# Optimization experiments

Measured on AMD Instinct MI355X. Metric: run time of the kernel, lower is better.

The kernel has to match this reference:

```python
import jax, jax.numpy as jnp
import numpy as np


def setup_inputs() -> dict:
    key = jax.random.key(0)
    ks = jax.random.split(key, 8)
    B, L, D, N, K = 4, 4096, 1024, 64, 4
    return {
        "x": jax.random.normal(ks[0], (B, L, D), dtype=jnp.float32),
        "conv_w": jax.random.normal(ks[1], (K, 1, D), dtype=jnp.float32) * 0.1,
        "conv_b": jnp.zeros((D,), dtype=jnp.float32),
        "Wp": jax.random.normal(ks[2], (D, 2 * N), dtype=jnp.float32) * (1.0 / np.sqrt(D)),
        "bp": jnp.zeros((2 * N,), dtype=jnp.float32),
        "Ws": jax.random.normal(ks[3], (D, N), dtype=jnp.float32) * (1.0 / np.sqrt(D)),
        "bs": jnp.zeros((N,), dtype=jnp.float32),
        "A_log": jax.random.normal(ks[4], (N,), dtype=jnp.float32) * 0.02,
        "dt_log": jax.random.normal(ks[5], (N,), dtype=jnp.float32) * 0.02,
        "Wo": jax.random.normal(ks[6], (N, D), dtype=jnp.float32) * (1.0 / np.sqrt(N)),
        "bo": jnp.zeros((D,), dtype=jnp.float32),
    }


def reference(x, conv_w, conv_b, Wp, bp, Ws, bs, A_log, dt_log, Wo, bo):
    B, L, D = x.shape
    K = conv_w.shape[0]
    N = Ws.shape[1]

    # causal depthwise conv: left-pad by K-1, sum K shifted slices (K is tiny)
    x_pad = jnp.pad(x, ((0, 0), (K - 1, 0), (0, 0)))
    conv = conv_b + sum(x_pad[:, k:k + L, :] * conv_w[k, 0] for k in range(K))

    proj = conv @ Wp + bp                     # [B, L, 2N]
    B_t = jax.nn.softplus(proj[..., :N])      # [B, L, N]
    C_t = jnp.tanh(proj[..., N:])             # [B, L, N]
    u = x @ Ws + bs                           # [B, L, N]

    A = -jax.nn.softplus(A_log)               # [N]
    dt = jax.nn.softplus(dt_log)              # [N]
    decay = 1.0 + dt * A                      # [N]

    def step(state, inputs):
        u_t, b_t, c_t = inputs                # each [B, N]
        state = decay * state + dt * b_t * u_t
        return state, c_t * state

    init = jnp.zeros((B, N), dtype=x.dtype)
    xs = tuple(jnp.swapaxes(a, 0, 1) for a in (u, B_t, C_t))  # time-major
    _, ys = jax.lax.scan(step, init, xs, unroll=4)            # [L, B, N]
    y = jnp.swapaxes(ys, 0, 1)                                # [B, L, N]
    return y @ Wo + bo                                        # [B, L, D]
```

## Files before the change

### kernel.cpp

```cpp
#include <hip/hip_runtime.h>

#define B_ 4
#define L_ 4096
#define D_ 1024
#define N_ 64

typedef _Float16 f16;
typedef __attribute__((ext_vector_type(8))) _Float16 half8;
typedef __attribute__((ext_vector_type(4))) float f32x4;

__device__ __forceinline__ float softplus_f(float x) {
    return fmaxf(x, 0.0f) + log1pf(__expf(-fabsf(x)));
}

__device__ __forceinline__ float tanh_f(float x) {
    float xc = fminf(fmaxf(x, -15.0f), 15.0f);
    float e = __expf(2.0f * xc);
    return (e - 1.0f) / (e + 1.0f);
}

__global__ __launch_bounds__(256) void k_prepw(
    const float* __restrict__ Wp, const float* __restrict__ Ws,
    const float* __restrict__ Wo, f16* __restrict__ WT, f16* __restrict__ WoT)
{
    int gid = blockIdx.x * 256 + threadIdx.x;
    if (gid < 24576) {
        int r = gid >> 7, kg = gid & 127;
        const float* src; int ncol, c;
        if (r < 128) { src = Wp; ncol = 128; c = r; }
        else         { src = Ws; ncol = 64;  c = r - 128; }
        f16 h[8];
        #pragma unroll
        for (int j = 0; j < 8; j++)
            h[j] = (f16)src[(size_t)(kg * 8 + j) * ncol + c];
        *(uint4*)&WT[(size_t)r * 1024 + kg * 8] = *(uint4*)h;
    } else {
        int g2 = gid - 24576;
        int d = g2 >> 3, ng = g2 & 7;
        f16 h[8];
        #pragma unroll
        for (int j = 0; j < 8; j++)
            h[j] = (f16)Wo[(size_t)(ng * 8 + j) * D_ + d];
        *(uint4*)&WoT[(size_t)d * 64 + ng * 8] = *(uint4*)h;
    }
}

__global__ __launch_bounds__(256) void k_frontend(
    const float* __restrict__ x, const float* __restrict__ conv_w,
    const float* __restrict__ conv_b, const f16* __restrict__ WT,
    const float* __restrict__ bp, const float* __restrict__ bs,
    const float* __restrict__ dt_log,
    f16* __restrict__ zT, f16* __restrict__ cT)
{
    __shared__ __align__(16) f16 xh[36 * 72];
    __shared__ float sE[3 * 32 * 68];

    const int tid = threadIdx.x;
    const int w = tid >> 6, lane = tid & 63;
    const int r = lane & 15, q = lane >> 4;
    const int T0 = blockIdx.x * 32;
    const int bb = T0 >> 12;
    const int l0 = T0 & (L_ - 1);
    const int cw0 = w * 48;

    f32x4 acc[3][2] = {};
    float4 rA[3];

    #define LDX(c0)                                                          \
        {                                                                    \
            _Pragma("unroll")                                                \
            for (int s = 0; s < 3; s++) {                                    \
                int idx = tid + 256 * s;                                     \
                float4 v = make_float4(0.f, 0.f, 0.f, 0.f);                  \
                if (idx < 576) {                                             \
                    int row = idx >> 4, g = idx & 15;                        \
                    int l = l0 + row - 4;                                    \
                    if (l >= 0)                                              \
                        v = *(const float4*)&x[((size_t)(bb * L_ + l)) * D_  \
                                               + (c0) + g * 4];              \
                }                                                            \
                rA[s] = v;                                                   \
            }                                                                \
        }

    LDX(0);
    for (int c = 0; c < 16; c++) {
        __syncthreads();
        #pragma unroll
        for (int s = 0; s < 3; s++) {
            int idx = tid + 256 * s;
            if (idx < 576) {
                int row = idx >> 4, g = idx & 15;
                f16 h[4] = {(f16)rA[s].x, (f16)rA[s].y, (f16)rA[s].z, (f16)rA[s].w};
                *(uint2*)&xh[row * 72 + g * 4] = *(uint2*)h;
            }
        }
        __syncthreads();
        if (c < 15) LDX((c + 1) * 64);

        const int k0 = c * 64;
        #pragma unroll
        for (int ks = 0; ks < 2; ks++) {
            const int kk = k0 + ks * 32 + q * 8;
            const int kl = ks * 32 + q * 8;

            half8 af[3];
            #pragma unroll
            for (int mf = 0; mf < 3; mf++)
                af[mf] = *(const half8*)&WT[(size_t)(cw0 + mf * 16 + r) * 1024 + kk];

            float cw3[8], cw2[8], cw1[8], cw0v[8], cbv[8];
            if (w < 3) {
                float4 a0 = *(const float4*)&conv_w[3 * D_ + kk];
                float4 a1 = *(const float4*)&conv_w[3 * D_ + kk + 4];
                float4 b0 = *(const float4*)&conv_w[2 * D_ + kk];
                float4 b1 = *(const float4*)&conv_w[2 * D_ + kk + 4];
                float4 c0v = *(const float4*)&conv_w[1 * D_ + kk];
                float4 c1v = *(const float4*)&conv_w[1 * D_ + kk + 4];
                float4 d0v = *(const float4*)&conv_w[0 * D_ + kk];
                float4 d1v = *(const float4*)&conv_w[0 * D_ + kk + 4];
                float4 e0 = *(const float4*)&conv_b[kk];
                float4 e1 = *(const float4*)&conv_b[kk + 4];
                cw3[0]=a0.x;cw3[1]=a0.y;cw3[2]=a0.z;cw3[3]=a0.w;cw3[4]=a1.x;cw3[5]=a1.y;cw3[6]=a1.z;cw3[7]=a1.w;
                cw2[0]=b0.x;cw2[1]=b0.y;cw2[2]=b0.z;cw2[3]=b0.w;cw2[4]=b1.x;cw2[5]=b1.y;cw2[6]=b1.z;cw2[7]=b1.w;
                cw1[0]=c0v.x;cw1[1]=c0v.y;cw1[2]=c0v.z;cw1[3]=c0v.w;cw1[4]=c1v.x;cw1[5]=c1v.y;cw1[6]=c1v.z;cw1[7]=c1v.w;
                cw0v[0]=d0v.x;cw0v[1]=d0v.y;cw0v[2]=d0v.z;cw0v[3]=d0v.w;cw0v[4]=d1v.x;cw0v[5]=d1v.y;cw0v[6]=d1v.z;cw0v[7]=d1v.w;
                cbv[0]=e0.x;cbv[1]=e0.y;cbv[2]=e0.z;cbv[3]=e0.w;cbv[4]=e1.x;cbv[5]=e1.y;cbv[6]=e1.z;cbv[7]=e1.w;
            }

            half8 braw[2], bcnv[2];
            #pragma unroll
            for (int nf = 0; nf < 2; nf++) {
                const int rb = nf * 16 + r + 4;
                half8 h0 = *(const half8*)&xh[rb * 72 + kl];
                braw[nf] = h0;
                if (w < 3) {
                    half8 h1 = *(const half8*)&xh[(rb - 1) * 72 + kl];
                    half8 h2 = *(const half8*)&xh[(rb - 2) * 72 + kl];
                    half8 h3 = *(const half8*)&xh[(rb - 3) * 72 + kl];
                    half8 hc;
                    #pragma unroll
                    for (int u = 0; u < 8; u++) {
                        float s0 = cbv[u];
                        s0 = fmaf(cw3[u], (float)h0[u], s0);
                        s0 = fmaf(cw2[u], (float)h1[u], s0);
                        s0 = fmaf(cw1[u], (float)h2[u], s0);
                        s0 = fmaf(cw0v[u], (float)h3[u], s0);
                        hc[u] = (f16)s0;
                    }
                    bcnv[nf] = hc;
                }
            }

            #pragma unroll
            for (int mf = 0; mf < 3; mf++) {
                const bool useConv = (cw0 + mf * 16) < 128;
                #pragma unroll
                for (int nf = 0; nf < 2; nf++)
                    acc[mf][nf] = __builtin_amdgcn_mfma_f32_16x16x32_f16(
                        af[mf], useConv ? bcnv[nf] : braw[nf], acc[mf][nf], 0, 0, 0);
            }
        }
    }

    float* sB = sE;
    float* sC = sE + 32 * 68;
    float* sU = sE + 2 * 32 * 68;
    __syncthreads();
    #pragma unroll
    for (int mf = 0; mf < 3; mf++) {
        const int cb4 = cw0 + mf * 16 + q * 4;
        const int seg = cb4 >> 6;
        const int cl = cb4 & 63;
        const float4 bb4 = (seg == 2) ? *(const float4*)&bs[cl]
                                      : *(const float4*)&bp[cb4];
        float* dst = (seg == 0) ? sB : (seg == 1 ? sC : sU);
        #pragma unroll
        for (int nf = 0; nf < 2; nf++) {
            const int t = nf * 16 + r;
            float v0 = acc[mf][nf][0] + bb4.x;
            float v1 = acc[mf][nf][1] + bb4.y;
            float v2 = acc[mf][nf][2] + bb4.z;
            float v3 = acc[mf][nf][3] + bb4.w;
            if (seg == 0) {
                v0 = softplus_f(v0); v1 = softplus_f(v1);
                v2 = softplus_f(v2); v3 = softplus_f(v3);
            } else if (seg == 1) {
                v0 = tanh_f(v0); v1 = tanh_f(v1);
                v2 = tanh_f(v2); v3 = tanh_f(v3);
            }
            float4 vv = {v0, v1, v2, v3};
            *(float4*)&dst[t * 68 + cl] = vv;
        }
    }
    __syncthreads();

    {
        const int n = tid >> 2, tg = tid & 3;
        const float dtv = softplus_f(dt_log[n]);
        f16 hz[8], hc[8];
        #pragma unroll
        for (int j = 0; j < 8; j++) {
            const int t = tg * 8 + j;
            hz[j] = (f16)(dtv * sB[t * 68 + n] * sU[t * 68 + n]);
            hc[j] = (f16)sC[t * 68 + n];
        }
        size_t o = ((size_t)(bb * N_ + n)) * L_ + l0 + tg * 8;
        *(uint4*)&zT[o] = *(uint4*)hz;
        *(uint4*)&cT[o] = *(uint4*)hc;
    }
    #undef LDX
}

__global__ __launch_bounds__(64) void k_scan(
    const f16* __restrict__ zT, const f16* __restrict__ cT,
    const float* __restrict__ A_log, const float* __restrict__ dt_log,
    f16* __restrict__ yH)
{
    __shared__ float zs[L_];
    __shared__ float cs[L_];
    const int bn = blockIdx.x;
    const int n = bn & (N_ - 1);
    const int lane = threadIdx.x;
    const f16* zp = zT + (size_t)bn * L_;
    const f16* cp = cT + (size_t)bn * L_;

    for (int it = 0; it < 8; it++) {
        int i = lane * 8 + it * 512;
        uint4 rz = *(const uint4*)(zp + i);
        uint4 rc = *(const uint4*)(cp + i);
        const f16* hz = (const f16*)&rz;
        const f16* hc = (const f16*)&rc;
        #pragma unroll
        for (int k = 0; k < 8; k++) {
            zs[i + k] = (float)hz[k];
            cs[i + k] = (float)hc[k];
        }
    }
    __syncthreads();

    float dtv = softplus_f(dt_log[n]);
    float Av = -softplus_f(A_log[n]);
    float dec = fmaf(dtv, Av, 1.0f);

    float s = 0.0f;
    const int base = lane * 64;
    #pragma unroll
    for (int j = 0; j < 64; j++) s = fmaf(dec, s, zs[base + j]);

    float d2 = dec * dec, d4 = d2 * d2, d8 = d4 * d4;
    float d16 = d8 * d8, d32 = d16 * d16, d64 = d32 * d32;

    float Ag = d64, Bg = s;
    #pragma unroll
    for (int off = 1; off < 64; off <<= 1) {
        float Ap = __shfl_up(Ag, off);
        float Bp = __shfl_up(Bg, off);
        if (lane >= off) { Bg = fmaf(Ag, Bp, Bg); Ag *= Ap; }
    }
    float carry = __shfl_up(Bg, 1);
    if (lane == 0) carry = 0.0f;

    float st = carry;
    #pragma unroll
    for (int j = 0; j < 64; j++) {
        st = fmaf(dec, st, zs[base + j]);
        zs[base + j] = cs[base + j] * st;
    }
    __syncthreads();
    f16* yp = yH + (size_t)bn * L_;
    for (int i = lane * 8; i < L_; i += 512) {
        f16 h[8];
        #pragma unroll
        for (int k = 0; k < 8; k++) h[k] = (f16)zs[i + k];
        *(uint4*)&yp[i] = *(uint4*)h;
    }
}

__global__ __launch_bounds__(256) void k_out(
    const f16* __restrict__ yH, const f16* __restrict__ WoT,
    const float* __restrict__ bo, float* __restrict__ out)
{
    __shared__ __align__(16) f16 ys[64 * 72];
    const int tid = threadIdx.x;
    const int w = tid >> 6, lane = tid & 63;
    const int r = lane & 15, q = lane >> 4;
    const int T0 = blockIdx.x * 64;
    const int bb = T0 >> 12, l0 = T0 & (L_ - 1);
    const int dw = blockIdx.y * 128 + w * 32;

    {
        const int n = tid & 63, tg = tid >> 6;
        #pragma unroll
        for (int h2 = 0; h2 < 2; h2++) {
            uint4 v = *(const uint4*)&yH[((size_t)(bb * N_ + n)) * L_ + l0 + tg * 16 + h2 * 8];
            const f16* hh = (const f16*)&v;
            #pragma unroll
            for (int j = 0; j < 8; j++)
                ys[(tg * 16 + h2 * 8 + j) * 72 + n] = hh[j];
        }
    }
    __syncthreads();

    f32x4 acc[2][4] = {};
    #pragma unroll
    for (int ks = 0; ks < 2; ks++) {
        const int kk = ks * 32 + q * 8;
        half8 af[2];
        #pragma unroll
        for (int mf = 0; mf < 2; mf++)
            af[mf] = *(const half8*)&WoT[(size_t)(dw + mf * 16 + r) * 64 + kk];
        #pragma unroll
        for (int nf = 0; nf < 4; nf++) {
            half8 bf = *(const half8*)&ys[(nf * 16 + r) * 72 + kk];
            #pragma unroll
            for (int mf = 0; mf < 2; mf++)
                acc[mf][nf] = __builtin_amdgcn_mfma_f32_16x16x32_f16(
                    af[mf], bf, acc[mf][nf], 0, 0, 0);
        }
    }

    #pragma unroll
    for (int mf = 0; mf < 2; mf++) {
        const int d = dw + mf * 16 + q * 4;
        const float4 bb4 = *(const float4*)&bo[d];
        #pragma unroll
        for (int nf = 0; nf < 4; nf++) {
            const int t = T0 + nf * 16 + r;
            float4 o = {acc[mf][nf][0] + bb4.x, acc[mf][nf][1] + bb4.y,
                        acc[mf][nf][2] + bb4.z, acc[mf][nf][3] + bb4.w};
            *(float4*)&out[(size_t)t * D_ + d] = o;
        }
    }
}

extern "C" void kernel_launch(void* const* d_in, const int* in_sizes, int n_in,
                              void* d_out, int out_size, void* d_ws, size_t ws_size,
                              hipStream_t stream) {
    const float* x      = (const float*)d_in[0];
    const float* conv_w = (const float*)d_in[1];
    const float* conv_b = (const float*)d_in[2];
    const float* Wp     = (const float*)d_in[3];
    const float* bp     = (const float*)d_in[4];
    const float* Ws     = (const float*)d_in[5];
    const float* bs     = (const float*)d_in[6];
    const float* A_log  = (const float*)d_in[7];
    const float* dt_log = (const float*)d_in[8];
    const float* Wo     = (const float*)d_in[9];
    const float* bo     = (const float*)d_in[10];
    float* out = (float*)d_out;

    char* wsp = (char*)d_ws;
    f16* WT  = (f16*)wsp;
    f16* WoT = (f16*)(wsp + 393216);
    f16* zT  = (f16*)(wsp + 524288);
    f16* cT  = (f16*)(wsp + 2621440);
    f16* yH  = (f16*)(wsp + 4718592);

    k_prepw<<<dim3(128), dim3(256), 0, stream>>>(Wp, Ws, Wo, WT, WoT);
    k_frontend<<<dim3(B_ * L_ / 32), dim3(256), 0, stream>>>(
        x, conv_w, conv_b, WT, bp, bs, dt_log, zT, cT);
    k_scan<<<dim3(B_ * N_), dim3(64), 0, stream>>>(zT, cT, A_log, dt_log, yH);
    k_out<<<dim3(B_ * L_ / 64, D_ / 128), dim3(256), 0, stream>>>(yH, WoT, bo, out);
}
```

Baseline: 201.2 us.

## Double-buffer frontend tiles, precompute conv once, parallelize scan across four waves

The frontend kernel now stages conv weights in shared memory. It computes the causal conv once per tile into a shared buffer instead of redundantly per wave, double-buffers the x tile, and prefetches weight fragments for the next chunk into registers. The scan kernel moves from one 64-thread wave with shared-memory staging to 256 threads that each hold 16 elements in registers, combining wave totals with a two-level parallel scan. The output kernel hoists its Wo fragment loads before the shared-memory staging. The changes add shared-memory and register pressure and raise the risk of precision loss in the powered decay terms.

```diff
diff --git a/kernel.cpp b/kernel.cpp
--- a/kernel.cpp
+++ b/kernel.cpp
@@ -52,7 +52,10 @@
     const float* __restrict__ dt_log,
     f16* __restrict__ zT, f16* __restrict__ cT)
 {
-    __shared__ __align__(16) f16 xh[36 * 72];
+    __shared__ float cwS[4 * 1024];
+    __shared__ float cbS[1024];
+    __shared__ __align__(16) f16 xh[2][36 * 72];
+    __shared__ __align__(16) f16 cvh[32 * 72];
     __shared__ float sE[3 * 32 * 68];
 
     const int tid = threadIdx.x;
@@ -65,6 +68,7 @@
 
     f32x4 acc[3][2] = {};
     float4 rA[3];
+    half8 wt[2][3][2];
 
     #define LDX(c0)                                                          \
         {                                                                    \
@@ -83,90 +87,111 @@
             }                                                                \
         }
 
+    #define STX(buf)                                                         \
+        {                                                                    \
+            _Pragma("unroll")                                                \
+            for (int s = 0; s < 3; s++) {                                    \
+                int idx = tid + 256 * s;                                     \
+                if (idx < 576) {                                             \
+                    int row = idx >> 4, g = idx & 15;                        \
+                    f16 h[4] = {(f16)rA[s].x, (f16)rA[s].y,                  \
+                                (f16)rA[s].z, (f16)rA[s].w};                 \
+                    *(uint2*)&xh[buf][row * 72 + g * 4] = *(uint2*)h;        \
+                }                                                            \
+            }                                                                \
+        }
+
+    #define LDWT(buf, cc)                                                    \
+        {                                                                    \
+            const int kb = (cc) * 64;                                        \
+            _Pragma("unroll")                                                \
+            for (int mf = 0; mf < 3; mf++)                                   \
+                _Pragma("unroll")                                            \
+                for (int ks = 0; ks < 2; ks++)                               \
+                    wt[buf][mf][ks] = *(const half8*)&WT[                    \
+                        (size_t)(cw0 + mf * 16 + r) * 1024 + kb + ks * 32 +  \
+                        q * 8];                                              \
+        }
+
+    for (int idx = tid; idx < 1024; idx += 256)
+        *(float4*)&cwS[idx * 4] = *(const float4*)&conv_w[idx * 4];
+    for (int idx = tid; idx < 256; idx += 256)
+        *(float4*)&cbS[idx * 4] = *(const float4*)&conv_b[idx * 4];
+
     LDX(0);
+    STX(0);
+    LDX(64);
+    LDWT(0, 0);
+    __syncthreads();
+
     for (int c = 0; c < 16; c++) {
+        const int cur = c & 1;
+        {
+            const int t = tid >> 3, kg = tid & 7;
+            const int kb = c * 64 + kg * 8;
+            float4 w3a = *(const float4*)&cwS[3 * 1024 + kb];
+            float4 w3b = *(const float4*)&cwS[3 * 1024 + kb + 4];
+            float4 w2a = *(const float4*)&cwS[2 * 1024 + kb];
+            float4 w2b = *(const float4*)&cwS[2 * 1024 + kb + 4];
+            float4 w1a = *(const float4*)&cwS[1 * 1024 + kb];
+            float4 w1b = *(const float4*)&cwS[1 * 1024 + kb + 4];
+            float4 w0a = *(const float4*)&cwS[0 * 1024 + kb];
+            float4 w0b = *(const float4*)&cwS[0 * 1024 + kb + 4];
+            float4 cba = *(const float4*)&cbS[kb];
+            float4 cbb = *(const float4*)&cbS[kb + 4];
+            half8 x0 = *(const half8*)&xh[cur][(t + 4) * 72 + kg * 8];
+            half8 x1 = *(const half8*)&xh[cur][(t + 3) * 72 + kg * 8];
+            half8 x2 = *(const half8*)&xh[cur][(t + 2) * 72 + kg * 8];
+            half8 x3 = *(const half8*)&xh[cur][(t + 1) * 72 + kg * 8];
+            float w3v[8] = {w3a.x,w3a.y,w3a.z,w3a.w,w3b.x,w3b.y,w3b.z,w3b.w};
+            float w2v[8] = {w2a.x,w2a.y,w2a.z,w2a.w,w2b.x,w2b.y,w2b.z,w2b.w};
+            float w1v[8] = {w1a.x,w1a.y,w1a.z,w1a.w,w1b.x,w1b.y,w1b.z,w1b.w};
+            float w0v[8] = {w0a.x,w0a.y,w0a.z,w0a.w,w0b.x,w0b.y,w0b.z,w0b.w};
+            float cbv[8] = {cba.x,cba.y,cba.z,cba.w,cbb.x,cbb.y,cbb.z,cbb.w};
+            half8 hc;
+            #pragma unroll
+            for (int u = 0; u < 8; u++) {
+                float s0 = cbv[u];
+                s0 = fmaf(w3v[u], (float)x0[u], s0);
+                s0 = fmaf(w2v[u], (float)x1[u], s0);
+                s0 = fmaf(w1v[u], (float)x2[u], s0);
+                s0 = fmaf(w0v[u], (float)x3[u], s0);
+                hc[u] = (f16)s0;
+            }
+            *(uint4*)&cvh[t * 72 + kg * 8] = *(uint4*)&hc;
+        }
         __syncthreads();
-        #pragma unroll
-        for (int s = 0; s < 3; s++) {
-            int idx = tid + 256 * s;
-            if (idx < 576) {
-                int row = idx >> 4, g = idx & 15;
-                f16 h[4] = {(f16)rA[s].x, (f16)rA[s].y, (f16)rA[s].z, (f16)rA[s].w};
-                *(uint2*)&xh[row * 72 + g * 4] = *(uint2*)h;
-            }
-        }
-        __syncthreads();
-        if (c < 15) LDX((c + 1) * 64);
-
-        const int k0 = c * 64;
+
+        if (c < 15) LDWT(1 - cur, c + 1);
+
         #pragma unroll
         for (int ks = 0; ks < 2; ks++) {
-            const int kk = k0 + ks * 32 + q * 8;
             const int kl = ks * 32 + q * 8;
-
-            half8 af[3];
-            #pragma unroll
-            for (int mf = 0; mf < 3; mf++)
-                af[mf] = *(const half8*)&WT[(size_t)(cw0 + mf * 16 + r) * 1024 + kk];
-
-            float cw3[8], cw2[8], cw1[8], cw0v[8], cbv[8];
-            if (w < 3) {
-                float4 a0 = *(const float4*)&conv_w[3 * D_ + kk];
-                float4 a1 = *(const float4*)&conv_w[3 * D_ + kk + 4];
-                float4 b0 = *(const float4*)&conv_w[2 * D_ + kk];
-                float4 b1 = *(const float4*)&conv_w[2 * D_ + kk + 4];
-                float4 c0v = *(const float4*)&conv_w[1 * D_ + kk];
-                float4 c1v = *(const float4*)&conv_w[1 * D_ + kk + 4];
-                float4 d0v = *(const float4*)&conv_w[0 * D_ + kk];
-                float4 d1v = *(const float4*)&conv_w[0 * D_ + kk + 4];
-                float4 e0 = *(const float4*)&conv_b[kk];
-                float4 e1 = *(const float4*)&conv_b[kk + 4];
-                cw3[0]=a0.x;cw3[1]=a0.y;cw3[2]=a0.z;cw3[3]=a0.w;cw3[4]=a1.x;cw3[5]=a1.y;cw3[6]=a1.z;cw3[7]=a1.w;
-                cw2[0]=b0.x;cw2[1]=b0.y;cw2[2]=b0.z;cw2[3]=b0.w;cw2[4]=b1.x;cw2[5]=b1.y;cw2[6]=b1.z;cw2[7]=b1.w;
-                cw1[0]=c0v.x;cw1[1]=c0v.y;cw1[2]=c0v.z;cw1[3]=c0v.w;cw1[4]=c1v.x;cw1[5]=c1v.y;cw1[6]=c1v.z;cw1[7]=c1v.w;
-                cw0v[0]=d0v.x;cw0v[1]=d0v.y;cw0v[2]=d0v.z;cw0v[3]=d0v.w;cw0v[4]=d1v.x;cw0v[5]=d1v.y;cw0v[6]=d1v.z;cw0v[7]=d1v.w;
-                cbv[0]=e0.x;cbv[1]=e0.y;cbv[2]=e0.z;cbv[3]=e0.w;cbv[4]=e1.x;cbv[5]=e1.y;cbv[6]=e1.z;cbv[7]=e1.w;
-            }
-
             half8 braw[2], bcnv[2];
             #pragma unroll
             for (int nf = 0; nf < 2; nf++) {
-                const int rb = nf * 16 + r + 4;
-                half8 h0 = *(const half8*)&xh[rb * 72 + kl];
-                braw[nf] = h0;
-                if (w < 3) {
-                    half8 h1 = *(const half8*)&xh[(rb - 1) * 72 + kl];
-                    half8 h2 = *(const half8*)&xh[(rb - 2) * 72 + kl];
-                    half8 h3 = *(const half8*)&xh[(rb - 3) * 72 + kl];
-                    half8 hc;
-                    #pragma unroll
-                    for (int u = 0; u < 8; u++) {
-                        float s0 = cbv[u];
-                        s0 = fmaf(cw3[u], (float)h0[u], s0);
-                        s0 = fmaf(cw2[u], (float)h1[u], s0);
-                        s0 = fmaf(cw1[u], (float)h2[u], s0);
-                        s0 = fmaf(cw0v[u], (float)h3[u], s0);
-                        hc[u] = (f16)s0;
-                    }
-                    bcnv[nf] = hc;
-                }
+                braw[nf] = *(const half8*)&xh[cur][(nf * 16 + r + 4) * 72 + kl];
+                bcnv[nf] = *(const half8*)&cvh[(nf * 16 + r) * 72 + kl];
             }
-
             #pragma unroll
             for (int mf = 0; mf < 3; mf++) {
                 const bool useConv = (cw0 + mf * 16) < 128;
                 #pragma unroll
                 for (int nf = 0; nf < 2; nf++)
                     acc[mf][nf] = __builtin_amdgcn_mfma_f32_16x16x32_f16(
-                        af[mf], useConv ? bcnv[nf] : braw[nf], acc[mf][nf], 0, 0, 0);
+                        wt[cur][mf][ks], useConv ? bcnv[nf] : braw[nf],
+                        acc[mf][nf], 0, 0, 0);
             }
         }
+
+        if (c < 15) STX(1 - cur);
+        if (c < 14) LDX((c + 2) * 64);
+        __syncthreads();
     }
 
     float* sB = sE;
     float* sC = sE + 32 * 68;
     float* sU = sE + 2 * 32 * 68;
-    __syncthreads();
     #pragma unroll
     for (int mf = 0; mf < 3; mf++) {
         const int cb4 = cw0 + mf * 16 + q * 4;
@@ -210,71 +235,88 @@
         *(uint4*)&cT[o] = *(uint4*)hc;
     }
     #undef LDX
-}
-
-__global__ __launch_bounds__(64) void k_scan(
+    #undef STX
+    #undef LDWT
+}
+
+__global__ __launch_bounds__(256) void k_scan(
     const f16* __restrict__ zT, const f16* __restrict__ cT,
     const float* __restrict__ A_log, const float* __restrict__ dt_log,
     f16* __restrict__ yH)
 {
-    __shared__ float zs[L_];
-    __shared__ float cs[L_];
+    __shared__ float Tw[4];
     const int bn = blockIdx.x;
     const int n = bn & (N_ - 1);
-    const int lane = threadIdx.x;
-    const f16* zp = zT + (size_t)bn * L_;
-    const f16* cp = cT + (size_t)bn * L_;
-
-    for (int it = 0; it < 8; it++) {
-        int i = lane * 8 + it * 512;
-        uint4 rz = *(const uint4*)(zp + i);
-        uint4 rc = *(const uint4*)(cp + i);
-        const f16* hz = (const f16*)&rz;
-        const f16* hc = (const f16*)&rc;
-        #pragma unroll
-        for (int k = 0; k < 8; k++) {
-            zs[i + k] = (float)hz[k];
-            cs[i + k] = (float)hc[k];
-        }
-    }
-    __syncthreads();
-
-    float dtv = softplus_f(dt_log[n]);
-    float Av = -softplus_f(A_log[n]);
-    float dec = fmaf(dtv, Av, 1.0f);
+    const int tid = threadIdx.x;
+    const int w = tid >> 6, lane = tid & 63;
+    const size_t base = (size_t)bn * L_ + tid * 16;
+
+    uint4 uz0 = *(const uint4*)(zT + base);
+    uint4 uz1 = *(const uint4*)(zT + base + 8);
+    uint4 uc0 = *(const uint4*)(cT + base);
+    uint4 uc1 = *(const uint4*)(cT + base + 8);
+
+    float z[16], cc[16];
+    {
+        const f16* hz0 = (const f16*)&uz0;
+        const f16* hz1 = (const f16*)&uz1;
+        const f16* hc0 = (const f16*)&uc0;
+        const f16* hc1 = (const f16*)&uc1;
+        #pragma unroll
+        for (int j = 0; j < 8; j++) {
+            z[j] = (float)hz0[j]; z[8 + j] = (float)hz1[j];
+            cc[j] = (float)hc0[j]; cc[8 + j] = (float)hc1[j];
+        }
+    }
+
+    const float dtv = softplus_f(dt_log[n]);
+    const float Av = -softplus_f(A_log[n]);
+    const float dec = fmaf(dtv, Av, 1.0f);
 
     float s = 0.0f;
-    const int base = lane * 64;
-    #pragma unroll
-    for (int j = 0; j < 64; j++) s = fmaf(dec, s, zs[base + j]);
-
-    float d2 = dec * dec, d4 = d2 * d2, d8 = d4 * d4;
-    float d16 = d8 * d8, d32 = d16 * d16, d64 = d32 * d32;
-
-    float Ag = d64, Bg = s;
+    #pragma unroll
+    for (int j = 0; j < 16; j++) s = fmaf(dec, s, z[j]);
+
+    const float d2 = dec * dec, d4 = d2 * d2, d8 = d4 * d4, a16 = d8 * d8;
+
+    float Ag = a16, Bg = s;
     #pragma unroll
     for (int off = 1; off < 64; off <<= 1) {
         float Ap = __shfl_up(Ag, off);
         float Bp = __shfl_up(Bg, off);
         if (lane >= off) { Bg = fmaf(Ag, Bp, Bg); Ag *= Ap; }
     }
-    float carry = __shfl_up(Bg, 1);
-    if (lane == 0) carry = 0.0f;
-
-    float st = carry;
-    #pragma unroll
-    for (int j = 0; j < 64; j++) {
-        st = fmaf(dec, st, zs[base + j]);
-        zs[base + j] = cs[base + j] * st;
-    }
+    float twv = __shfl(Bg, 63);
+    if (lane == 0) Tw[w] = twv;
     __syncthreads();
-    f16* yp = yH + (size_t)bn * L_;
-    for (int i = lane * 8; i < L_; i += 512) {
-        f16 h[8];
-        #pragma unroll
-        for (int k = 0; k < 8; k++) h[k] = (f16)zs[i + k];
-        *(uint4*)&yp[i] = *(uint4*)h;
-    }
+
+    float a32 = a16 * a16, a64 = a32 * a32, a128 = a64 * a64;
+    float a256 = a128 * a128, a512 = a256 * a256, a1024 = a512 * a512;
+
+    float S = 0.0f;
+    for (int v = 0; v < w; v++) S = fmaf(a1024, S, Tw[v]);
+
+    float cl = __shfl_up(Bg, 1);
+    if (lane == 0) cl = 0.0f;
+
+    float p = 1.0f, bpow = a16;
+    int e = lane;
+    #pragma unroll
+    for (int bit = 0; bit < 6; bit++) {
+        if (e & 1) p *= bpow;
+        bpow *= bpow;
+        e >>= 1;
+    }
+
+    float st = fmaf(S, p, cl);
+    f16 hy[16];
+    #pragma unroll
+    for (int j = 0; j < 16; j++) {
+        st = fmaf(dec, st, z[j]);
+        hy[j] = (f16)(cc[j] * st);
+    }
+    *(uint4*)(yH + base) = *(uint4*)&hy[0];
+    *(uint4*)(yH + base + 8) = *(uint4*)&hy[8];
 }
 
 __global__ __launch_bounds__(256) void k_out(
@@ -289,11 +331,20 @@
     const int bb = T0 >> 12, l0 = T0 & (L_ - 1);
     const int dw = blockIdx.y * 128 + w * 32;
 
+    half8 af[2][2];
+    #pragma unroll
+    for (int ks = 0; ks < 2; ks++)
+        #pragma unroll
+        for (int mf = 0; mf < 2; mf++)
+            af[ks][mf] = *(const half8*)&WoT[(size_t)(dw + mf * 16 + r) * 64 +
+                                             ks * 32 + q * 8];
+
     {
         const int n = tid & 63, tg = tid >> 6;
         #pragma unroll
         for (int h2 = 0; h2 < 2; h2++) {
-            uint4 v = *(const uint4*)&yH[((size_t)(bb * N_ + n)) * L_ + l0 + tg * 16 + h2 * 8];
+            uint4 v = *(const uint4*)&yH[((size_t)(bb * N_ + n)) * L_ + l0 +
+                                         tg * 16 + h2 * 8];
             const f16* hh = (const f16*)&v;
             #pragma unroll
             for (int j = 0; j < 8; j++)
@@ -306,17 +357,13 @@
     #pragma unroll
     for (int ks = 0; ks < 2; ks++) {
         const int kk = ks * 32 + q * 8;
-        half8 af[2];
-        #pragma unroll
-        for (int mf = 0; mf < 2; mf++)
-            af[mf] = *(const half8*)&WoT[(size_t)(dw + mf * 16 + r) * 64 + kk];
         #pragma unroll
         for (int nf = 0; nf < 4; nf++) {
             half8 bf = *(const half8*)&ys[(nf * 16 + r) * 72 + kk];
             #pragma unroll
             for (int mf = 0; mf < 2; mf++)
                 acc[mf][nf] = __builtin_amdgcn_mfma_f32_16x16x32_f16(
-                    af[mf], bf, acc[mf][nf], 0, 0, 0);
+                    af[ks][mf], bf, acc[mf][nf], 0, 0, 0);
         }
     }
 
@@ -360,6 +407,6 @@
     k_prepw<<<dim3(128), dim3(256), 0, stream>>>(Wp, Ws, Wo, WT, WoT);
     k_frontend<<<dim3(B_ * L_ / 32), dim3(256), 0, stream>>>(
         x, conv_w, conv_b, WT, bp, bs, dt_log, zT, cT);
-    k_scan<<<dim3(B_ * N_), dim3(64), 0, stream>>>(zT, cT, A_log, dt_log, yH);
+    k_scan<<<dim3(B_ * N_), dim3(256), 0, stream>>>(zT, cT, A_log, dt_log, yH);
     k_out<<<dim3(B_ * L_ / 64, D_ / 128), dim3(256), 0, stream>>>(yH, WoT, bo, out);
 }
```

Result: slower. 236.0 us (+17.3%).
